# Kernel optimization log

Measured on AMD Instinct MI355X. Metric: run time of the kernel, lower is better.

The kernel has to match this reference:

```python
import jax, jax.numpy as jnp
import numpy as np

N_NODES = 50000
N_EDGES = 800000
IN_DIM = 128
HIDDEN = 128


def setup_inputs() -> dict:
    key = jax.random.key(0)
    ks = jax.random.split(key, 8)
    feat = jax.random.normal(ks[0], (N_NODES, IN_DIM), dtype=jnp.float32)
    hx = jax.random.normal(ks[1], (N_NODES, HIDDEN), dtype=jnp.float32)
    src = jax.random.randint(ks[2], (N_EDGES,), 0, N_NODES, dtype=jnp.int32)
    dst = jax.random.randint(ks[3], (N_EDGES,), 0, N_NODES, dtype=jnp.int32)
    s_i = 1.0 / np.sqrt(IN_DIM)
    s_h = 1.0 / np.sqrt(HIDDEN)
    W_i = jax.random.uniform(ks[4], (IN_DIM, 3 * HIDDEN), jnp.float32, -s_i, s_i)
    b_i = jnp.zeros((3 * HIDDEN,), jnp.float32)
    W_h = jax.random.uniform(ks[5], (HIDDEN, 3 * HIDDEN), jnp.float32, -s_h, s_h)
    b_h = jnp.zeros((3 * HIDDEN,), jnp.float32)
    return {"feat": feat, "hx": hx, "W_i": W_i, "b_i": b_i,
            "W_h": W_h, "b_h": b_h, "src": src, "dst": dst}


def _graph_conv(x, W, b, src, dst, norm_src, norm_dst):
    # DGL GraphConv, norm='both', in_feats < out_feats path:
    # scale by out-degree^{-1/2} of src, aggregate-sum to dst,
    # scale by in-degree^{-1/2} of dst, then linear.
    x = x * norm_src[:, None]                      # [N, d]
    agg = jax.ops.segment_sum(x[src], dst, num_segments=N_NODES)  # [N, d]
    agg = agg * norm_dst[:, None]
    return agg @ W + b                             # [N, 3*hidden]


def reference(feat, hx, W_i, b_i, W_h, b_h, src, dst):
    ones = jnp.ones((src.shape[0],), jnp.float32)
    deg_out = jax.ops.segment_sum(ones, src, num_segments=N_NODES)
    deg_in = jax.ops.segment_sum(ones, dst, num_segments=N_NODES)
    norm_src = jax.lax.rsqrt(jnp.clip(deg_out, 1.0))
    norm_dst = jax.lax.rsqrt(jnp.clip(deg_in, 1.0))

    i = _graph_conv(feat, W_i, b_i, src, dst, norm_src, norm_dst)
    h = _graph_conv(hx, W_h, b_h, src, dst, norm_src, norm_dst)

    i_r, i_z, i_n = jnp.split(i, 3, axis=-1)
    h_r, h_z, h_n = jnp.split(h, 3, axis=-1)
    r = jax.nn.sigmoid(i_r + h_r)
    z = jax.nn.sigmoid(i_z + h_z)
    n = jnp.tanh(i_n + r * h_n)
    return (1.0 - z) * n + z * hx
```

## Files before the change

kernel.cpp:

```cpp
#include <hip/hip_runtime.h>
#include <math.h>

#define DIM 128
#define NCH 32
#define RGMAX 6272

typedef float f32x4v __attribute__((ext_vector_type(4)));
typedef short bf16x8 __attribute__((ext_vector_type(8)));

static __device__ __forceinline__ short f2bf(float f) {
    unsigned u = __float_as_uint(f);
    unsigned r = (u + 0x7fffu + ((u >> 16) & 1u)) >> 16;
    return (short)r;
}
static __device__ __forceinline__ float bf2f(unsigned short s) {
    return __uint_as_float(((unsigned)s) << 16);
}

__global__ __launch_bounds__(256) void k_hist(const int* __restrict__ src,
                                              const int* __restrict__ dst,
                                              int* __restrict__ partO,
                                              int* __restrict__ partI,
                                              int* __restrict__ rank,
                                              int N, int E, int chunk, int rgsz) {
    __shared__ int hO[RGMAX], hI[RGMAX];
    int t = threadIdx.x;
    int c = blockIdx.x % NCH, r = blockIdx.x / NCH;
    int lo = r * rgsz;
    int hi = min(lo + rgsz, N);
    for (int i = t; i < rgsz; i += 256) { hO[i] = 0; hI[i] = 0; }
    __syncthreads();
    int e0 = c * chunk, e1 = min(e0 + chunk, E);
    for (int e = e0 + t; e < e1; e += 256) {
        int s = src[e], d = dst[e];
        if (s >= lo && s < hi) atomicAdd(&hO[s - lo], 1);
        if (d >= lo && d < hi) rank[e] = atomicAdd(&hI[d - lo], 1);
    }
    __syncthreads();
    for (int i = t; i < hi - lo; i += 256) {
        partO[(size_t)c * N + lo + i] = hO[i];
        partI[(size_t)c * N + lo + i] = hI[i];
    }
}

__global__ __launch_bounds__(256) void k_bsum(const int* __restrict__ partI,
                                              int* __restrict__ bsum, int N) {
    __shared__ int red[4];
    int b = blockIdx.x, t = threadIdx.x;
    int n = b * 256 + t;
    int s = 0;
    if (n < N) {
        #pragma unroll
        for (int c = 0; c < NCH; ++c) s += partI[(size_t)c * N + n];
    }
    for (int off = 32; off; off >>= 1) s += __shfl_down(s, off);
    if ((t & 63) == 0) red[t >> 6] = s;
    __syncthreads();
    if (t == 0) bsum[b] = red[0] + red[1] + red[2] + red[3];
}

__global__ __launch_bounds__(256) void k_off(const int* __restrict__ partI,
                                             int* partO_csrC,
                                             const int* __restrict__ bsum,
                                             int* __restrict__ csrOff,
                                             float* __restrict__ normIf,
                                             float* __restrict__ normOf,
                                             int N, int NB) {
    __shared__ int sp[256];
    __shared__ int sbase;
    int b = blockIdx.x, t = threadIdx.x;
    int own = (t < NB) ? bsum[t] : 0;
    sp[t] = own;
    __syncthreads();
    for (int off = 1; off < 256; off <<= 1) {
        int u = (t >= off) ? sp[t - off] : 0;
        __syncthreads();
        sp[t] += u;
        __syncthreads();
    }
    if (t == b) sbase = sp[t] - own;
    if (b == 0 && t == NB - 1) csrOff[N] = sp[t];
    __syncthreads();
    int n = b * 256 + t;
    int cv[NCH];
    int tI = 0, tO = 0;
    if (n < N) {
        #pragma unroll
        for (int c = 0; c < NCH; ++c) {
            cv[c] = partI[(size_t)c * N + n];
            tI += cv[c];
            tO += partO_csrC[(size_t)c * N + n];
        }
    }
    sp[t] = tI;
    __syncthreads();
    for (int off = 1; off < 256; off <<= 1) {
        int u = (t >= off) ? sp[t - off] : 0;
        __syncthreads();
        sp[t] += u;
        __syncthreads();
    }
    int o = sbase + sp[t] - tI;
    if (n < N) {
        csrOff[n] = o;
        normIf[n] = rsqrtf(fmaxf((float)tI, 1.0f));
        normOf[n] = rsqrtf(fmaxf((float)tO, 1.0f));
        int base = o;
        #pragma unroll
        for (int c = 0; c < NCH; ++c) {
            partO_csrC[(size_t)c * N + n] = base;
            base += cv[c];
        }
    }
}

__global__ __launch_bounds__(256) void k_xcw(const float* __restrict__ feat,
                                             const float* __restrict__ hx,
                                             const float* __restrict__ Wi,
                                             const float* __restrict__ Wh,
                                             const float* __restrict__ normOf,
                                             short* __restrict__ Wbf,
                                             short* __restrict__ fh,
                                             const int* __restrict__ src,
                                             const int* __restrict__ dst,
                                             const int* __restrict__ rank,
                                             const int* __restrict__ csrOffC,
                                             int* __restrict__ srcSorted,
                                             int N, int E, int chunk) {
    int i = blockIdx.x * 256 + threadIdx.x;
    int T1 = N * 64;
    int T2 = T1 + 98304;
    if (i < T1) {
        int n = i >> 6, q = i & 63;
        float ns = normOf[n];
        const float* spp = (q < 32) ? &feat[(size_t)n * 128 + q * 4]
                                    : &hx[(size_t)n * 128 + (q - 32) * 4];
        float4 v = *(const float4*)spp;
        short4 p;
        p.x = f2bf(v.x * ns); p.y = f2bf(v.y * ns);
        p.z = f2bf(v.z * ns); p.w = f2bf(v.w * ns);
        *(short4*)&fh[(size_t)n * 256 + q * 4] = p;
    } else if (i < T2) {
        int w = i - T1;
        int k = w & 127, n = (w >> 7) & 15, r = w >> 11;
        int gm = r % 6, cb = r / 6;
        const float* Wsrc = (gm < 3) ? Wi : Wh;
        int g = gm % 3;
        Wbf[w] = f2bf(Wsrc[k * 384 + g * 128 + cb * 16 + n]);
    } else {
        int e = i - T2;
        if (e < E) {
            int c = e / chunk;
            int pos = csrOffC[(size_t)c * N + dst[e]] + rank[e];
            srcSorted[pos] = src[e];
        }
    }
}

__global__ __launch_bounds__(256) void gather_kernel(
    const short* __restrict__ fh, const int* __restrict__ csrOff,
    const int* __restrict__ srcSorted, const float* __restrict__ normIf,
    short* __restrict__ agg, int N) {
    int wv = threadIdx.x >> 6, lane = threadIdx.x & 63;
    int d = blockIdx.x * 4 + wv;
    if (d >= N) return;
    const ushort4* fh4 = (const ushort4*)fh;
    int beg = csrOff[d], end = csrOff[d + 1];
    float4 acc = make_float4(0.f, 0.f, 0.f, 0.f);
    #pragma unroll 8
    for (int e = beg; e < end; ++e) {
        int s = srcSorted[e];
        ushort4 v = fh4[(size_t)s * 64 + lane];
        acc.x += bf2f(v.x); acc.y += bf2f(v.y);
        acc.z += bf2f(v.z); acc.w += bf2f(v.w);
    }
    float nd = normIf[d];
    short4 p;
    p.x = f2bf(acc.x * nd); p.y = f2bf(acc.y * nd);
    p.z = f2bf(acc.z * nd); p.w = f2bf(acc.w * nd);
    *(short4*)&agg[(size_t)d * 256 + lane * 4] = p;
}

#define GLOAD_LDS16(gp, lp)                                                   \
    __builtin_amdgcn_global_load_lds(                                         \
        (const __attribute__((address_space(1))) void*)(gp),                  \
        (__attribute__((address_space(3))) void*)(lp), 16, 0, 0)

__global__ __launch_bounds__(256, 3) void gemm_gates_kernel(
    const short* __restrict__ agg, const float* __restrict__ hx,
    const short* __restrict__ Wbf,
    const float* __restrict__ bi, const float* __restrict__ bh,
    float* __restrict__ out, int N) {
    __shared__ short wlds[2][12288];
    const int tid = threadIdx.x;
    const int wv = tid >> 6, lane = tid & 63;
    const int l15 = lane & 15, quad = lane >> 4;
    const int rowBase = (blockIdx.x * 4 + wv) * 16;
    const bool active = rowBase < N;

    int arow = active ? rowBase + l15 : 0;
    const short* aPtr = agg + (size_t)arow * 256;
    bf16x8 aLo[4], aHi[4];
    #pragma unroll
    for (int kst = 0; kst < 4; ++kst) {
        aLo[kst] = *(const bf16x8*)&aPtr[kst * 32 + quad * 8];
        aHi[kst] = *(const bf16x8*)&aPtr[128 + kst * 32 + quad * 8];
    }

    {
        const char* gs = (const char*)Wbf;
        #pragma unroll
        for (int i = 0; i < 6; ++i) {
            int ldsByte = wv * 6144 + i * 1024 + lane * 16;
            int gByte = ldsByte ^ (((ldsByte >> 8) & 15) << 4);
            GLOAD_LDS16(gs + gByte, (char*)&wlds[0][0] + wv * 6144 + i * 1024);
        }
    }
    __syncthreads();

    for (int cb = 0; cb < 8; ++cb) {
        const int buf = cb & 1;
        if (cb < 7) {
            const char* gs = (const char*)(Wbf + (size_t)(cb + 1) * 12288);
            #pragma unroll
            for (int i = 0; i < 6; ++i) {
                int ldsByte = wv * 6144 + i * 1024 + lane * 16;
                int gByte = ldsByte ^ (((ldsByte >> 8) & 15) << 4);
                GLOAD_LDS16(gs + gByte,
                            (char*)&wlds[buf ^ 1][0] + wv * 6144 + i * 1024);
            }
        }
        if (active) {
            f32x4v acc[6];
            #pragma unroll
            for (int g = 0; g < 6; ++g) acc[g] = (f32x4v){0.f, 0.f, 0.f, 0.f};
            const char* slab = (const char*)&wlds[buf][0];
            #pragma unroll
            for (int kst = 0; kst < 4; ++kst) {
                const int co = (((kst * 4 + quad) ^ l15) << 4);
                #pragma unroll
                for (int g = 0; g < 3; ++g) {
                    bf16x8 bI = *(const bf16x8*)(slab + g * 4096 + l15 * 256 + co);
                    acc[g] = __builtin_amdgcn_mfma_f32_16x16x32_bf16(
                        aLo[kst], bI, acc[g], 0, 0, 0);
                    bf16x8 bH = *(const bf16x8*)(slab + (g + 3) * 4096 + l15 * 256 + co);
                    acc[g + 3] = __builtin_amdgcn_mfma_f32_16x16x32_bf16(
                        aHi[kst], bH, acc[g + 3], 0, 0, 0);
                }
            }
            int ocol = cb * 16 + l15;
            float bir = bi[ocol], biz = bi[128 + ocol], bin = bi[256 + ocol];
            float bhr = bh[ocol], bhz = bh[128 + ocol], bhn = bh[256 + ocol];
            #pragma unroll
            for (int reg = 0; reg < 4; ++reg) {
                int row = rowBase + quad * 4 + reg;
                float ir = acc[0][reg] + bir, iz = acc[1][reg] + biz, in_ = acc[2][reg] + bin;
                float hr = acc[3][reg] + bhr, hz = acc[4][reg] + bhz, hn = acc[5][reg] + bhn;
                float rg = 1.0f / (1.0f + __expf(-(ir + hr)));
                float zg = 1.0f / (1.0f + __expf(-(iz + hz)));
                float ng = tanhf(in_ + rg * hn);
                float hv = hx[(size_t)row * DIM + ocol];
                out[(size_t)row * DIM + ocol] = (1.0f - zg) * ng + zg * hv;
            }
        }
        __syncthreads();
    }
}

extern "C" void kernel_launch(void* const* d_in, const int* in_sizes, int n_in,
                              void* d_out, int out_size, void* d_ws, size_t ws_size,
                              hipStream_t stream) {
    const float* feat = (const float*)d_in[0];
    const float* hx   = (const float*)d_in[1];
    const float* Wi   = (const float*)d_in[2];
    const float* bi   = (const float*)d_in[3];
    const float* Wh   = (const float*)d_in[4];
    const float* bh   = (const float*)d_in[5];
    const int* src    = (const int*)d_in[6];
    const int* dst    = (const int*)d_in[7];
    float* out        = (float*)d_out;

    int N = in_sizes[0] / DIM;
    int E = in_sizes[6];
    int rgsz  = (N + 7) / 8;
    int nrg   = (N + rgsz - 1) / rgsz;
    int chunk = (E + NCH - 1) / NCH;
    int NB    = (N + 255) / 256;

    int* wsi = (int*)d_ws;
    int* partI     = wsi;
    int* partO     = wsi + (size_t)NCH * N;
    int* csrOff    = wsi + (size_t)2 * NCH * N;
    int* srcSorted = csrOff + N + 1;
    int* rank      = srcSorted + E;
    int* bsum      = rank + E;
    float* normIf  = (float*)(bsum + 256);
    float* normOf  = normIf + N;
    size_t iend = (size_t)(2 * NCH * N + N + 1 + 2 * E + 256 + 2 * N);
    size_t wofs = (iend * 4 + 15) & ~(size_t)15;
    short* Wbf = (short*)((char*)d_ws + wofs);
    size_t fofs = (wofs + 98304 * 2 + 15) & ~(size_t)15;
    short* fh = (short*)((char*)d_ws + fofs);
    short* agg = (short*)d_out;

    k_hist<<<NCH * nrg, 256, 0, stream>>>(src, dst, partO, partI, rank,
                                          N, E, chunk, rgsz);
    k_bsum<<<NB, 256, 0, stream>>>(partI, bsum, N);
    k_off<<<NB, 256, 0, stream>>>(partI, partO, bsum, csrOff,
                                  normIf, normOf, N, NB);
    k_xcw<<<(N * 64 + 98304 + E + 255) / 256, 256, 0, stream>>>(
        feat, hx, Wi, Wh, normOf, Wbf, fh,
        src, dst, rank, partO , srcSorted, N, E, chunk);

    gather_kernel<<<(N + 3) / 4, 256, 0, stream>>>(
        fh, csrOff, srcSorted, normIf, agg, N);
    gemm_gates_kernel<<<(N + 63) / 64, 256, 0, stream>>>(
        agg, hx, Wbf, bi, bh, out, N);
}
```

Baseline: 276.0 us.

## Pack degree histograms as 16-bit counters in LDS and split in/out blocks

The histogram kernel no longer loops over 8 node ranges per edge chunk. It now keeps a full-graph histogram in shared memory by packing two 16-bit counters into each 32-bit word, and uses separate blocks for in-degree and out-degree. The per-chunk partial counts and the ranks are stored as unsigned shorts, which halves their memory traffic, and a separate csrOffC buffer is added. This removes the 8x redundant reads of src/dst. The cost is only 64 blocks of 1024 threads, which may underuse the GPU, plus the risk of 16-bit overflow if a single chunk holds more than 65535 edges to one node.

New measurement: 251.0 us. -9.1%, faster.

```diff
diff --git a/kernel.cpp b/kernel.cpp
--- a/kernel.cpp
+++ b/kernel.cpp
@@ -3,7 +3,7 @@
 
 #define DIM 128
 #define NCH 32
-#define RGMAX 6272
+#define NMAXW 25024
 
 typedef float f32x4v __attribute__((ext_vector_type(4)));
 typedef short bf16x8 __attribute__((ext_vector_type(8)));
@@ -17,41 +17,47 @@
     return __uint_as_float(((unsigned)s) << 16);
 }
 
-__global__ __launch_bounds__(256) void k_hist(const int* __restrict__ src,
-                                              const int* __restrict__ dst,
-                                              int* __restrict__ partO,
-                                              int* __restrict__ partI,
-                                              int* __restrict__ rank,
-                                              int N, int E, int chunk, int rgsz) {
-    __shared__ int hO[RGMAX], hI[RGMAX];
+__global__ __launch_bounds__(1024) void k_hist(const int* __restrict__ src,
+                                               const int* __restrict__ dst,
+                                               unsigned short* __restrict__ partO,
+                                               unsigned short* __restrict__ partI,
+                                               unsigned short* __restrict__ rank,
+                                               int N, int Npad, int E, int chunk) {
+    __shared__ unsigned int h[NMAXW];
     int t = threadIdx.x;
-    int c = blockIdx.x % NCH, r = blockIdx.x / NCH;
-    int lo = r * rgsz;
-    int hi = min(lo + rgsz, N);
-    for (int i = t; i < rgsz; i += 256) { hO[i] = 0; hI[i] = 0; }
+    int isI = blockIdx.x < NCH;
+    int c = isI ? blockIdx.x : blockIdx.x - NCH;
+    int NW = (N + 1) >> 1;
+    for (int i = t; i < NW; i += 1024) h[i] = 0;
     __syncthreads();
     int e0 = c * chunk, e1 = min(e0 + chunk, E);
-    for (int e = e0 + t; e < e1; e += 256) {
-        int s = src[e], d = dst[e];
-        if (s >= lo && s < hi) atomicAdd(&hO[s - lo], 1);
-        if (d >= lo && d < hi) rank[e] = atomicAdd(&hI[d - lo], 1);
-    }
-    __syncthreads();
-    for (int i = t; i < hi - lo; i += 256) {
-        partO[(size_t)c * N + lo + i] = hO[i];
-        partI[(size_t)c * N + lo + i] = hI[i];
-    }
-}
-
-__global__ __launch_bounds__(256) void k_bsum(const int* __restrict__ partI,
-                                              int* __restrict__ bsum, int N) {
+    if (isI) {
+        for (int e = e0 + t; e < e1; e += 1024) {
+            int d = dst[e];
+            unsigned sh = (d & 1) * 16;
+            unsigned old = atomicAdd(&h[d >> 1], 1u << sh);
+            rank[e] = (unsigned short)((old >> sh) & 0xffffu);
+        }
+    } else {
+        for (int e = e0 + t; e < e1; e += 1024) {
+            int s = src[e];
+            atomicAdd(&h[s >> 1], 1u << ((s & 1) * 16));
+        }
+    }
+    __syncthreads();
+    unsigned int* p = (unsigned int*)((isI ? partI : partO) + (size_t)c * Npad);
+    for (int i = t; i < NW; i += 1024) p[i] = h[i];
+}
+
+__global__ __launch_bounds__(256) void k_bsum(const unsigned short* __restrict__ partI,
+                                              int* __restrict__ bsum, int N, int Npad) {
     __shared__ int red[4];
     int b = blockIdx.x, t = threadIdx.x;
     int n = b * 256 + t;
     int s = 0;
     if (n < N) {
         #pragma unroll
-        for (int c = 0; c < NCH; ++c) s += partI[(size_t)c * N + n];
+        for (int c = 0; c < NCH; ++c) s += partI[(size_t)c * Npad + n];
     }
     for (int off = 32; off; off >>= 1) s += __shfl_down(s, off);
     if ((t & 63) == 0) red[t >> 6] = s;
@@ -59,13 +65,14 @@
     if (t == 0) bsum[b] = red[0] + red[1] + red[2] + red[3];
 }
 
-__global__ __launch_bounds__(256) void k_off(const int* __restrict__ partI,
-                                             int* partO_csrC,
+__global__ __launch_bounds__(256) void k_off(const unsigned short* __restrict__ partI,
+                                             const unsigned short* __restrict__ partO,
                                              const int* __restrict__ bsum,
+                                             int* __restrict__ csrOffC,
                                              int* __restrict__ csrOff,
                                              float* __restrict__ normIf,
                                              float* __restrict__ normOf,
-                                             int N, int NB) {
+                                             int N, int Npad, int NB) {
     __shared__ int sp[256];
     __shared__ int sbase;
     int b = blockIdx.x, t = threadIdx.x;
@@ -87,9 +94,9 @@
     if (n < N) {
         #pragma unroll
         for (int c = 0; c < NCH; ++c) {
-            cv[c] = partI[(size_t)c * N + n];
+            cv[c] = partI[(size_t)c * Npad + n];
             tI += cv[c];
-            tO += partO_csrC[(size_t)c * N + n];
+            tO += partO[(size_t)c * Npad + n];
         }
     }
     sp[t] = tI;
@@ -108,7 +115,7 @@
         int base = o;
         #pragma unroll
         for (int c = 0; c < NCH; ++c) {
-            partO_csrC[(size_t)c * N + n] = base;
+            csrOffC[(size_t)c * N + n] = base;
             base += cv[c];
         }
     }
@@ -123,7 +130,7 @@
                                              short* __restrict__ fh,
                                              const int* __restrict__ src,
                                              const int* __restrict__ dst,
-                                             const int* __restrict__ rank,
+                                             const unsigned short* __restrict__ rank,
                                              const int* __restrict__ csrOffC,
                                              int* __restrict__ srcSorted,
                                              int N, int E, int chunk) {
@@ -151,7 +158,7 @@
         int e = i - T2;
         if (e < E) {
             int c = e / chunk;
-            int pos = csrOffC[(size_t)c * N + dst[e]] + rank[e];
+            int pos = csrOffC[(size_t)c * N + dst[e]] + (int)rank[e];
             srcSorted[pos] = src[e];
         }
     }
@@ -282,35 +289,34 @@
 
     int N = in_sizes[0] / DIM;
     int E = in_sizes[6];
-    int rgsz  = (N + 7) / 8;
-    int nrg   = (N + rgsz - 1) / rgsz;
+    int Npad = (N + 1) & ~1;
     int chunk = (E + NCH - 1) / NCH;
     int NB    = (N + 255) / 256;
 
-    int* wsi = (int*)d_ws;
-    int* partI     = wsi;
-    int* partO     = wsi + (size_t)NCH * N;
-    int* csrOff    = wsi + (size_t)2 * NCH * N;
+    unsigned short* partI = (unsigned short*)d_ws;
+    unsigned short* partO = partI + (size_t)NCH * Npad;
+    int* csrOffC   = (int*)(partO + (size_t)NCH * Npad);
+    int* csrOff    = csrOffC + (size_t)NCH * N;
     int* srcSorted = csrOff + N + 1;
-    int* rank      = srcSorted + E;
-    int* bsum      = rank + E;
+    unsigned short* rank = (unsigned short*)(srcSorted + E);
+    int* bsum      = (int*)(rank + ((E + 1) & ~1));
     float* normIf  = (float*)(bsum + 256);
     float* normOf  = normIf + N;
-    size_t iend = (size_t)(2 * NCH * N + N + 1 + 2 * E + 256 + 2 * N);
+    size_t iend = (size_t)(normOf + N - (float*)d_ws);
     size_t wofs = (iend * 4 + 15) & ~(size_t)15;
     short* Wbf = (short*)((char*)d_ws + wofs);
     size_t fofs = (wofs + 98304 * 2 + 15) & ~(size_t)15;
     short* fh = (short*)((char*)d_ws + fofs);
     short* agg = (short*)d_out;
 
-    k_hist<<<NCH * nrg, 256, 0, stream>>>(src, dst, partO, partI, rank,
-                                          N, E, chunk, rgsz);
-    k_bsum<<<NB, 256, 0, stream>>>(partI, bsum, N);
-    k_off<<<NB, 256, 0, stream>>>(partI, partO, bsum, csrOff,
-                                  normIf, normOf, N, NB);
+    k_hist<<<2 * NCH, 1024, 0, stream>>>(src, dst, partO, partI, rank,
+                                         N, Npad, E, chunk);
+    k_bsum<<<NB, 256, 0, stream>>>(partI, bsum, N, Npad);
+    k_off<<<NB, 256, 0, stream>>>(partI, partO, bsum, csrOffC, csrOff,
+                                  normIf, normOf, N, Npad, NB);
     k_xcw<<<(N * 64 + 98304 + E + 255) / 256, 256, 0, stream>>>(
         feat, hx, Wi, Wh, normOf, Wbf, fh,
-        src, dst, rank, partO , srcSorted, N, E, chunk);
+        src, dst, rank, csrOffC, srcSorted, N, E, chunk);
 
     gather_kernel<<<(N + 3) / 4, 256, 0, stream>>>(
         fh, csrOff, srcSorted, normIf, agg, N);
```
